# Performance work log

Measured on AMD Instinct MI355X. Metric: run time of the kernel, lower is better.

## Reference

```python
import jax, jax.numpy as jnp
import numpy as np

GR = 16

def _conv(x, w, b, pad):
    y = jax.lax.conv_general_dilated(x, w, (1, 1), [(pad, pad), (pad, pad)],
                                     dimension_numbers=('NCHW', 'OIHW', 'NCHW'))
    return y + b[None, :, None, None]

def _build_stencil(h, w):
    num = h * w
    a = np.zeros((num, 4, num), np.float32)
    i = np.arange(num)
    m0 = ((i + 1) % w != 0) & (i + 1 < num)
    a[i[m0], 0, i[m0]] = 1.0; a[i[m0], 0, i[m0] + 1] = -1.0
    m1 = i + w < num
    a[i[m1], 1, i[m1]] = 1.0; a[i[m1], 1, i[m1] + w] = -1.0
    m2 = ((i + 2) % w != 0) & (i + 2 < num)
    a[i[m2], 2, i[m2]] = 1.0; a[i[m2], 2, i[m2] + 2] = -1.0
    m3 = i + 2 * w < num
    a[i[m3], 3, i[m3]] = 1.0; a[i[m3], 3, i[m3] + 2 * w] = -1.0
    a[-1, 0, -1] = 1.0; a[-1, 1, -1] = 1.0; a[-1, 2, -1] = 1.0; a[-1, 3, -1] = 1.0
    return jnp.asarray(a)  # (num, 4, num)

def setup_inputs() -> dict:
    key = jax.random.key(0)
    ks = jax.random.split(key, 20)
    n, c, h, w = 4, 64, 24, 24
    s = 0.02
    inp = {
        'x': jax.random.normal(ks[0], (n, c, h, w), jnp.float32),
        'a': _build_stencil(h, w),
        'grad_w1': jax.random.normal(ks[1], (c, c, 3, 3)) * s,
        'grad_b1': jnp.zeros((c,)),
        'grad_w2': jax.random.normal(ks[2], (4 * GR, c, 3, 3)) * s,
        'grad_b2': jnp.zeros((4 * GR,)),
        'att_w1': jax.random.normal(ks[3], (c, c, 3, 3)) * s,
        'att_b1': jnp.zeros((c,)),
        'att_w2': jax.random.normal(ks[4], (4 * GR, c, 3, 3)) * s,
        'att_b2': jnp.zeros((4 * GR,)),
        'se_w1': jax.random.normal(ks[5], (c // 2, c, 1, 1)) * s,
        'se_b1': jnp.zeros((c // 2,)),
        'se_w2': jax.random.normal(ks[6], (GR, c // 2, 1, 1)) * s,
        'se_b2': jnp.zeros((GR,)),
        'gn_w': jnp.ones((GR,)),
        'gn_b': jnp.zeros((GR,)),
        'post_w': jax.random.normal(ks[7], (8 * GR, GR, 3, 3)) * s,
        'post_b': jnp.zeros((8 * GR,)),
    }
    return inp

def reference(x, a, grad_w1, grad_b1, grad_w2, grad_b2,
              att_w1, att_b1, att_w2, att_b2,
              se_w1, se_b1, se_w2, se_b2,
              gn_w, gn_b, post_w, post_b):
    n, c, h, w = x.shape
    num = h * w
    # attention branch: conv -> leaky_relu -> conv -> sigmoid
    att = jax.nn.sigmoid(_conv(jax.nn.leaky_relu(_conv(x, att_w1, att_b1, 1), 0.01), att_w2, att_b2, 1))
    # gradient branch: conv -> leaky_relu -> conv
    grad = _conv(jax.nn.leaky_relu(_conv(x, grad_w1, grad_b1, 1), 0.01), grad_w2, grad_b2, 1)
    # squeeze-excite: GAP -> 1x1 conv -> leaky -> 1x1 conv -> sigmoid
    pooled = x.mean(axis=(2, 3), keepdims=True)  # (n,c,1,1)
    se = jax.nn.sigmoid(_conv(jax.nn.leaky_relu(_conv(pooled, se_w1, se_b1, 0), 0.01), se_w2, se_b2, 0))
    # reshape per-pixel 4-tap weights: (n*GR, num, 4, 1)
    att_r = att.reshape(n * GR, 4, num, 1).transpose(0, 2, 1, 3)
    grad_r = grad.reshape(n * GR, 4, num, 1).transpose(0, 2, 1, 3)
    # densified weighted stencil operator
    A = a[None] * att_r                      # (b, num, 4, num)
    B = (grad_r * att_r)[..., 0]             # (b, num, 4)
    A = A.reshape(n * GR, num * 4, num)      # (b, 4num, num)
    B = B.reshape(n * GR, num * 4)           # (b, 4num)
    ATA = jnp.einsum('bkn,bkm->bnm', A, A)   # (b, num, num)
    ATB = jnp.einsum('bkn,bk->bn', A, B)[..., None]
    ATA = ATA + jnp.eye(num, dtype=x.dtype)[None] * 1e-12
    sol = jnp.linalg.solve(ATA, ATB)         # (b, num, 1)
    y = sol.reshape(n, GR, h, w)
    # GroupNorm(1, GR): normalize over all channels + spatial, eps=1e-5
    mu = y.mean(axis=(1, 2, 3), keepdims=True)
    var = y.var(axis=(1, 2, 3), keepdims=True)
    y = (y - mu) / jnp.sqrt(var + 1e-5)
    y = y * gn_w[None, :, None, None] + gn_b[None, :, None, None]
    y = se * y
    return _conv(y, post_w, post_b, 1)
```

## Files before the change

### kernel.cpp

```cpp
#include <hip/hip_runtime.h>
#include <math.h>

#define NUM 576
#define BSTR 50
#define CTH 512
#define CHOL_LDS_BYTES ((NUM * BSTR + CTH) * sizeof(float))

__device__ __forceinline__ float leakyf(float v) { return v > 0.f ? v : 0.01f * v; }
__device__ __forceinline__ float sigmoidf(float v) { return 1.f / (1.f + __expf(-v)); }
__device__ __forceinline__ float rdlane(float v, int l) {
  return __uint_as_float(__builtin_amdgcn_readlane(__float_as_uint(v), l));
}

__global__ __launch_bounds__(576) void conv1se_kernel(
    const float* __restrict__ x,
    const float* __restrict__ wa, const float* __restrict__ ba,
    const float* __restrict__ wg, const float* __restrict__ bg,
    const float* __restrict__ sw1, const float* __restrict__ sb1,
    const float* __restrict__ sw2, const float* __restrict__ sb2,
    float* __restrict__ outa, float* __restrict__ outg,
    float* __restrict__ sev, double* __restrict__ acc)
{
  __shared__ float sx[16 * 676];
  __shared__ float pooled[64];
  __shared__ float hid[32];
  const int co = blockIdx.x, n = blockIdx.y;
  const int tid = threadIdx.x;

  if (co == 64) {
    if (tid < 2) acc[n * 2 + tid] = 0.0;
    if (tid < 64) {
      const float4* xp4 = (const float4*)(x + (size_t)(n * 64 + tid) * 576);
      float s = 0.f;
      for (int p = 0; p < 144; ++p) {
        float4 v = xp4[p];
        s += v.x + v.y + v.z + v.w;
      }
      pooled[tid] = s * (1.f / 576.f);
    }
    __syncthreads();
    if (tid < 32) {
      float h = sb1[tid];
      for (int c = 0; c < 64; ++c) h += pooled[c] * sw1[tid * 64 + c];
      hid[tid] = leakyf(h);
    }
    __syncthreads();
    if (tid < 16) {
      float v = sb2[tid];
      for (int j = 0; j < 32; ++j) v += hid[j] * sw2[tid * 32 + j];
      sev[n * 16 + tid] = sigmoidf(v);
    }
    return;
  }

  const int py = tid / 24, px = tid - py * 24;
  const int hb0 = py * 26 + px;
  for (int i = tid; i < 16 * 676; i += 576) sx[i] = 0.f;
  float acc_a = ba[co];
  float acc_g = bg[co];
  for (int c0 = 0; c0 < 64; c0 += 16) {
    __syncthreads();
#pragma unroll
    for (int q = 0; q < 4; ++q) {
      const int p = tid + q * 576;
      const int k = p / 144;
      const int r = p - k * 144;
      const int pix = r * 4;
      const int ppy = pix / 24, ppx = pix - ppy * 24;
      const float4 v = *(const float4*)&x[(size_t)(n * 64 + c0) * 576 + p * 4];
      float* d = &sx[k * 676 + (ppy + 1) * 26 + ppx + 1];
      d[0] = v.x; d[1] = v.y; d[2] = v.z; d[3] = v.w;
    }
    __syncthreads();
#pragma unroll 4
    for (int k = 0; k < 16; ++k) {
      const float* wpa = wa + (co * 64 + c0 + k) * 9;
      const float* wpg = wg + (co * 64 + c0 + k) * 9;
      const float* sp = &sx[k * 676 + hb0];
#pragma unroll
      for (int dy = 0; dy < 3; ++dy)
#pragma unroll
        for (int dx = 0; dx < 3; ++dx) {
          const float v = sp[dy * 26 + dx];
          acc_a += v * wpa[dy * 3 + dx];
          acc_g += v * wpg[dy * 3 + dx];
        }
    }
  }
  const int o = (n * 64 + co) * 576 + tid;
  outa[o] = leakyf(acc_a);
  outg[o] = leakyf(acc_g);
}

__global__ __launch_bounds__(576) void conv2_kernel(
    const float* __restrict__ t1a, const float* __restrict__ t1g,
    const float* __restrict__ wa, const float* __restrict__ ba,
    const float* __restrict__ wg, const float* __restrict__ bg,
    float* __restrict__ att, float* __restrict__ grd)
{
  __shared__ float sx[16 * 676];
  const int co = blockIdx.x, n = blockIdx.y, br = blockIdx.z;
  const float* src = br ? t1g : t1a;
  const float* wp0 = br ? wg : wa;
  const float bias = br ? bg[co] : ba[co];
  float* dst = br ? grd : att;
  const int tid = threadIdx.x;
  const int py = tid / 24, px = tid - py * 24;
  const int hb0 = py * 26 + px;
  for (int i = tid; i < 16 * 676; i += 576) sx[i] = 0.f;
  float acc = bias;
  for (int c0 = 0; c0 < 64; c0 += 16) {
    __syncthreads();
#pragma unroll
    for (int q = 0; q < 4; ++q) {
      const int p = tid + q * 576;
      const int k = p / 144;
      const int r = p - k * 144;
      const int pix = r * 4;
      const int ppy = pix / 24, ppx = pix - ppy * 24;
      const float4 v = *(const float4*)&src[(size_t)(n * 64 + c0) * 576 + p * 4];
      float* d = &sx[k * 676 + (ppy + 1) * 26 + ppx + 1];
      d[0] = v.x; d[1] = v.y; d[2] = v.z; d[3] = v.w;
    }
    __syncthreads();
#pragma unroll 4
    for (int k = 0; k < 16; ++k) {
      const float* wp = wp0 + (co * 64 + c0 + k) * 9;
      const float* sp = &sx[k * 676 + hb0];
#pragma unroll
      for (int dy = 0; dy < 3; ++dy)
#pragma unroll
        for (int dx = 0; dx < 3; ++dx)
          acc += sp[dy * 26 + dx] * wp[dy * 3 + dx];
    }
  }
  if (br == 0) acc = sigmoidf(acc);
  dst[(n * 64 + co) * 576 + tid] = acc;
}

__device__ __forceinline__ void scale_panel_f(
    float* __restrict__ S, float* RHS_s, float* RD_s, float (*CP)[64],
    float* DUMW, int t, int j, int maxrow, int dumidx)
{
  const int row = j + t;
  const bool rok = row <= maxrow;
  float v[8];
#pragma unroll
  for (int c = 0; c < 8; ++c) {
    const bool okc = rok && (t >= c) && (t - c <= 48);
    const int addr = okc ? (row * BSTR + (t - c)) : dumidx;
    float vv = S[addr];
    v[c] = okc ? vv : 0.f;
  }
  float zb[8];
#pragma unroll
  for (int k = 0; k < 8; ++k) zb[k] = RHS_s[j + k];
  float z = RHS_s[rok ? row : j];
  z = rok ? z : 0.f;
  float rdv[8], y[8], lp[8][8];
#pragma unroll
  for (int k = 0; k < 8; ++k) {
    if (k == 0) rdv[0] = RD_s[j];
    else rdv[k] = rsqrtf(rdlane(v[k], k));
    v[k] *= rdv[k];
#pragma unroll
    for (int m = k + 1; m < 8; ++m) {
      lp[m][k] = rdlane(v[k], m);
      v[m] -= v[k] * lp[m][k];
    }
  }
  y[0] = zb[0] * rdv[0];
#pragma unroll
  for (int k = 1; k < 8; ++k) {
    float a = zb[k];
#pragma unroll
    for (int m = 0; m < 8; ++m)
      if (m < k) a -= lp[k][m] * y[m];
    y[k] = a * rdv[k];
  }
  float zn = z;
#pragma unroll
  for (int c = 0; c < 8; ++c) zn -= v[c] * y[c];
#pragma unroll
  for (int c = 0; c < 8; ++c) {
    const bool okc = rok && (t > c) && (t - c <= 48);
    float* bp = okc ? &S[row * BSTR + (t - c)] : &S[dumidx];
    *bp = v[c];
    CP[c][t] = okc ? v[c] : 0.f;
  }
  if (t < 8) {
    float yv = y[0], rv = rdv[0];
#pragma unroll
    for (int k = 1; k < 8; ++k) {
      yv = (t == k) ? y[k] : yv;
      rv = (t == k) ? rdv[k] : rv;
    }
    RHS_s[row] = yv;
    RD_s[row] = rv;
  } else {
    float* rp = rok ? &RHS_s[row] : &DUMW[t & 63];
    *rp = zn;
  }
}

__device__ __forceinline__ void scale_panel_b(
    float* __restrict__ S, float* RHS_s, float* RD_s, float (*CP)[64],
    float* DUMW, int t, int jf, int dumidx)
{
  const int rr = jf + t;
  const bool rok = rr <= 287;
  float v[8];
#pragma unroll
  for (int c = 0; c < 8; ++c) {
    const bool okc = rok && (t >= c) && (t - c <= 48);
    const int addr = okc ? ((575 - rr + (t - c)) * BSTR + (t - c)) : dumidx;
    float vv = S[addr];
    v[c] = okc ? vv : 0.f;
  }
  float zb[8];
#pragma unroll
  for (int k = 0; k < 8; ++k) zb[k] = RHS_s[575 - (jf + k)];
  float z = RHS_s[rok ? (575 - rr) : (575 - jf)];
  z = rok ? z : 0.f;
  float rdv[8], y[8], lp[8][8];
#pragma unroll
  for (int k = 0; k < 8; ++k) {
    if (k == 0) rdv[0] = RD_s[575 - jf];
    else rdv[k] = rsqrtf(rdlane(v[k], k));
    v[k] *= rdv[k];
#pragma unroll
    for (int m = k + 1; m < 8; ++m) {
      lp[m][k] = rdlane(v[k], m);
      v[m] -= v[k] * lp[m][k];
    }
  }
  y[0] = zb[0] * rdv[0];
#pragma unroll
  for (int k = 1; k < 8; ++k) {
    float a = zb[k];
#pragma unroll
    for (int m = 0; m < 8; ++m)
      if (m < k) a -= lp[k][m] * y[m];
    y[k] = a * rdv[k];
  }
  float zn = z;
#pragma unroll
  for (int c = 0; c < 8; ++c) zn -= v[c] * y[c];
#pragma unroll
  for (int c = 0; c < 8; ++c) {
    const bool okc = rok && (t > c) && (t - c <= 48);
    float* bp = okc ? &S[(575 - rr + (t - c)) * BSTR + (t - c)] : &S[dumidx];
    *bp = v[c];
    CP[c][t] = okc ? v[c] : 0.f;
  }
  if (t < 8) {
    float yv = y[0], rv = rdv[0];
#pragma unroll
    for (int k = 1; k < 8; ++k) {
      yv = (t == k) ? y[k] : yv;
      rv = (t == k) ? rdv[k] : rv;
    }
    RHS_s[575 - rr] = yv;
    RD_s[575 - rr] = rv;
  } else {
    float* rp = rok ? &RHS_s[575 - rr] : &DUMW[t & 63];
    *rp = zn;
  }
}

__global__ __launch_bounds__(CTH, 1) void chol_kernel(
    const float* __restrict__ att, const float* __restrict__ grd,
    float* __restrict__ sol, double* __restrict__ acc)
{
  extern __shared__ float S[];
  __shared__ float RHS_s[NUM];
  __shared__ float RD_s[NUM];
  __shared__ float XS_s[NUM];
  __shared__ __align__(16) float CPF[8][64];
  __shared__ __align__(16) float CPB[8][64];
  __shared__ float DUMW[64];
  __shared__ double RW[16];
  const int b = blockIdx.x, tid = threadIdx.x;
  const int n = b >> 4, g = b & 15;
  const float* ac = att + (size_t)(n * 64 + g * 4) * 576;
  const float* gc = grd + (size_t)(n * 64 + g * 4) * 576;
  const int dumidx = NUM * BSTR + tid;

  int r1A, r2A, r1B, r2B;
  const bool okA = tid < 300;
  const int btid = (tid >= 300) ? (tid - 300) : ((tid < 88) ? (tid + 212) : -1);
  const bool okB = btid >= 0;
  {
    int T = okA ? tid : 0;
    int U = (int)((sqrtf(8.f * (float)T + 1.f) - 1.f) * 0.5f);
    while (U * (U + 1) / 2 > T) --U;
    while ((U + 1) * (U + 2) / 2 <= T) ++U;
    int W = T - U * (U + 1) / 2;
    r1A = 8 + 2 * U; r2A = 8 + 2 * W;
    T = okB ? btid : 0;
    U = (int)((sqrtf(8.f * (float)T + 1.f) - 1.f) * 0.5f);
    while (U * (U + 1) / 2 > T) --U;
    while ((U + 1) * (U + 2) / 2 <= T) ++U;
    W = T - U * (U + 1) / 2;
    r1B = 8 + 2 * U; r2B = 8 + 2 * W;
  }

  for (int i = tid; i < NUM * BSTR; i += CTH) S[i] = 0.f;
  __syncthreads();

  for (int i = tid; i < NUM; i += CTH) {
    float diag = 1e-12f, rv = 0.f;
    float od1 = 0.f, od2 = 0.f, od24 = 0.f, od48 = 0.f;
    if (((i + 1) % 24 != 0) && (i + 1 < NUM)) {
      float a0 = ac[0 * 576 + i]; float s = a0 * a0;
      diag += s; rv += s * gc[0 * 576 + i];
    }
    if (i - 1 >= 0 && (i % 24 != 0)) {
      float a0 = ac[0 * 576 + (i - 1)]; float s = a0 * a0;
      diag += s; rv -= s * gc[0 * 576 + (i - 1)]; od1 = -s;
    }
    if (i + 24 < NUM) {
      float a1 = ac[1 * 576 + i]; float s = a1 * a1;
      diag += s; rv += s * gc[1 * 576 + i];
    }
    if (i - 24 >= 0) {
      float a1 = ac[1 * 576 + (i - 24)]; float s = a1 * a1;
      diag += s; rv -= s * gc[1 * 576 + (i - 24)]; od24 = -s;
    }
    if (((i + 2) % 24 != 0) && (i + 2 < NUM)) {
      float a2 = ac[2 * 576 + i]; float s = a2 * a2;
      diag += s; rv += s * gc[2 * 576 + i];
    }
    if (i - 2 >= 0 && (i % 24 != 0)) {
      float a2 = ac[2 * 576 + (i - 2)]; float s = a2 * a2;
      diag += s; rv -= s * gc[2 * 576 + (i - 2)]; od2 = -s;
    }
    if (i + 48 < NUM) {
      float a3 = ac[3 * 576 + i]; float s = a3 * a3;
      diag += s; rv += s * gc[3 * 576 + i];
    }
    if (i - 48 >= 0) {
      float a3 = ac[3 * 576 + (i - 48)]; float s = a3 * a3;
      diag += s; rv -= s * gc[3 * 576 + (i - 48)]; od48 = -s;
    }
    if (i == NUM - 1) {
#pragma unroll
      for (int t = 0; t < 4; ++t) {
        float a = ac[t * 576 + (NUM - 1)]; float s = a * a;
        diag += s; rv += s * gc[t * 576 + (NUM - 1)];
      }
    }
    S[i * BSTR + 0] = diag;
    S[i * BSTR + 1] = od1;
    S[i * BSTR + 2] = od2;
    S[i * BSTR + 24] = od24;
    S[i * BSTR + 48] = od48;
    RHS_s[i] = rv;
    if (i == 0) RD_s[0] = rsqrtf(diag);
    if (i == NUM - 1) RD_s[NUM - 1] = rsqrtf(diag);
  }

  for (int s = 0; s < 30; ++s) {
    const int j = 8 * s;
    __syncthreads();
    const int pF = j * BSTR + 51 * r1A - r2A;
    float* qF00 = okA ? &S[pF] : &S[dumidx];
    float* qF01 = okA ? &S[pF - 1] : &S[dumidx];
    float* qF10 = okA ? &S[pF + 51] : &S[dumidx];
    float* qF11 = okA ? &S[pF + 50] : &S[dumidx];
    const int pB = (575 - j - r2B) * BSTR + (r1B - r2B);
    float* qB00 = okB ? &S[pB] : &S[dumidx];
    float* qB01 = okB ? &S[pB - 51] : &S[dumidx];
    float* qB10 = okB ? &S[pB + 1] : &S[dumidx];
    float* qB11 = okB ? &S[pB - 50] : &S[dumidx];
    const float vF00 = *qF00, vF01 = *qF01, vF10 = *qF10, vF11 = *qF11;
    const float vB00 = *qB00, vB01 = *qB01, vB10 = *qB10, vB11 = *qB11;
    if (tid < 64)
      scale_panel_f(S, RHS_s, RD_s, CPF, DUMW, tid, j, 287, dumidx);
    else if (tid < 128)
      scale_panel_b(S, RHS_s, RD_s, CPB, DUMW, tid - 64, j, dumidx);
    __syncthreads();
    {
      float2 cr[8], cc[8];
#pragma unroll
      for (int c = 0; c < 8; ++c) {
        cr[c] = *(const float2*)&CPF[c][r1A];
        cc[c] = *(const float2*)&CPF[c][r2A];
      }
      float s00 = 0.f, s01 = 0.f, s10 = 0.f, s11 = 0.f;
#pragma unroll
      for (int c = 0; c < 8; ++c) {
        s00 += cr[c].x * cc[c].x; s01 += cr[c].x * cc[c].y;
        s10 += cr[c].y * cc[c].x; s11 += cr[c].y * cc[c].y;
      }
      const float t00 = vF00 - s00;
      *qF00 = t00; *qF01 = vF01 - s01;
      *qF10 = vF10 - s10; *qF11 = vF11 - s11;
      if (tid == 0) RD_s[j + 8] = rsqrtf(t00);
    }
    {
      float2 cr[8], cc[8];
#pragma unroll
      for (int c = 0; c < 8; ++c) {
        cr[c] = *(const float2*)&CPB[c][r1B];
        cc[c] = *(const float2*)&CPB[c][r2B];
      }
      float s00 = 0.f, s01 = 0.f, s10 = 0.f, s11 = 0.f;
#pragma unroll
      for (int c = 0; c < 8; ++c) {
        s00 += cr[c].x * cc[c].x; s01 += cr[c].x * cc[c].y;
        s10 += cr[c].y * cc[c].x; s11 += cr[c].y * cc[c].y;
      }
      const float t00 = vB00 - s00;
      *qB00 = t00; *qB01 = vB01 - s01;
      *qB10 = vB10 - s10; *qB11 = vB11 - s11;
      if (btid == 0 && j + 8 <= 239) RD_s[575 - (j + 8)] = rsqrtf(t00);
    }
  }

  for (int j = 240; j < 336; j += 8) {
    __syncthreads();
    const int R = 335 - j;
    const bool a0 = okA && (r1A <= R);
    const bool a1 = okA && (r1A + 1 <= R);
    const int pM = j * BSTR + 51 * r1A - r2A;
    float* qM00 = a0 ? &S[pM] : &S[dumidx];
    float* qM01 = a0 ? &S[pM - 1] : &S[dumidx];
    float* qM10 = a1 ? &S[pM + 51] : &S[dumidx];
    float* qM11 = a1 ? &S[pM + 50] : &S[dumidx];
    const float vM00 = *qM00, vM01 = *qM01, vM10 = *qM10, vM11 = *qM11;
    if (tid < 64)
      scale_panel_f(S, RHS_s, RD_s, CPF, DUMW, tid, j, 335, dumidx);
    __syncthreads();
    {
      float2 cr[8], cc[8];
#pragma unroll
      for (int c = 0; c < 8; ++c) {
        cr[c] = *(const float2*)&CPF[c][r1A];
        cc[c] = *(const float2*)&CPF[c][r2A];
      }
      float s00 = 0.f, s01 = 0.f, s10 = 0.f, s11 = 0.f;
#pragma unroll
      for (int c = 0; c < 8; ++c) {
        s00 += cr[c].x * cc[c].x; s01 += cr[c].x * cc[c].y;
        s10 += cr[c].y * cc[c].x; s11 += cr[c].y * cc[c].y;
      }
      const float t00 = vM00 - s00;
      *qM00 = t00; *qM01 = vM01 - s01;
      *qM10 = vM10 - s10; *qM11 = vM11 - s11;
      if (tid == 0 && a0) RD_s[j + 8] = rsqrtf(t00);
    }
  }
  __syncthreads();

  if (tid < 64) {
    const int t = tid;
    for (int i = 335; i >= 247; i -= 8) {
      asm volatile("s_waitcnt lgkmcnt(0)" ::: "memory");
      float zz[8], rr2[8];
#pragma unroll
      for (int k = 0; k < 8; ++k) { zz[k] = RHS_s[i - k]; rr2[k] = RD_s[i - k]; }
      float L[8][8];
#pragma unroll
      for (int a = 0; a < 8; ++a)
#pragma unroll
        for (int bb = 0; bb < 8; ++bb)
          if (bb > a) L[a][bb] = S[(i - a) * BSTR + (bb - a)];
      float x[8];
      x[0] = zz[0] * rr2[0];
#pragma unroll
      for (int k = 1; k < 8; ++k) {
        float a2 = zz[k];
#pragma unroll
        for (int m = 0; m < 8; ++m)
          if (m < k) a2 -= L[m][k] * x[m];
        x[k] = a2 * rr2[k];
      }
      const int rb = i - 8 - t;
      const bool bok = rb >= 0;
      float acc2 = 0.f;
#pragma unroll
      for (int k = 0; k < 8; ++k) {
        const int d = 8 + t - k;
        const bool ok = bok && (d <= 48);
        float Lv = S[ok ? ((i - k) * BSTR + d) : dumidx];
        Lv = ok ? Lv : 0.f;
        acc2 += Lv * x[k];
      }
      const float zbv = RHS_s[bok ? rb : 0];
      float* rp = bok ? &RHS_s[rb] : &DUMW[t];
      *rp = zbv - acc2;
      float xv = x[0];
#pragma unroll
      for (int k = 1; k < 8; ++k) xv = (t == k) ? x[k] : xv;
      if (t < 8) XS_s[i - t] = xv;
    }
  }
  __syncthreads();

  if (tid < 48) {
    const int jj = 336 + tid;
    float sacc = 0.f;
    for (int i = jj - 48; i <= 335; ++i)
      sacc += S[jj * BSTR + (jj - i)] * XS_s[i];
    RHS_s[jj] -= sacc;
  }
  __syncthreads();

  if (tid < 64) {
    const int t = tid;
    for (int i = 239; i >= 7; i -= 8) {
      asm volatile("s_waitcnt lgkmcnt(0)" ::: "memory");
      float zz[8], rr2[8];
#pragma unroll
      for (int k = 0; k < 8; ++k) { zz[k] = RHS_s[i - k]; rr2[k] = RD_s[i - k]; }
      float L[8][8];
#pragma unroll
      for (int a = 0; a < 8; ++a)
#pragma unroll
        for (int bb = 0; bb < 8; ++bb)
          if (bb > a) L[a][bb] = S[(i - a) * BSTR + (bb - a)];
      float x[8];
      x[0] = zz[0] * rr2[0];
#pragma unroll
      for (int k = 1; k < 8; ++k) {
        float a2 = zz[k];
#pragma unroll
        for (int m = 0; m < 8; ++m)
          if (m < k) a2 -= L[m][k] * x[m];
        x[k] = a2 * rr2[k];
      }
      const int rb = i - 8 - t;
      const bool bok = rb >= 0;
      float acc2 = 0.f;
#pragma unroll
      for (int k = 0; k < 8; ++k) {
        const int d = 8 + t - k;
        const bool ok = bok && (d <= 48);
        float Lv = S[ok ? ((i - k) * BSTR + d) : dumidx];
        Lv = ok ? Lv : 0.f;
        acc2 += Lv * x[k];
      }
      const float zbv = RHS_s[bok ? rb : 0];
      float* rp = bok ? &RHS_s[rb] : &DUMW[t];
      *rp = zbv - acc2;
      float xv = x[0];
#pragma unroll
      for (int k = 1; k < 8; ++k) xv = (t == k) ? x[k] : xv;
      if (t < 8) XS_s[i - t] = xv;
    }
  } else if (tid < 128) {
    const int t = tid - 64;
    for (int i = 239; i >= 7; i -= 8) {
      asm volatile("s_waitcnt lgkmcnt(0)" ::: "memory");
      float zz[8], rr2[8];
#pragma unroll
      for (int k = 0; k < 8; ++k) {
        zz[k] = RHS_s[575 - (i - k)];
        rr2[k] = RD_s[575 - (i - k)];
      }
      float L[8][8];
#pragma unroll
      for (int a = 0; a < 8; ++a)
#pragma unroll
        for (int bb = 0; bb < 8; ++bb)
          if (bb > a) L[a][bb] = S[(575 - (i - bb)) * BSTR + (bb - a)];
      float x[8];
      x[0] = zz[0] * rr2[0];
#pragma unroll
      for (int k = 1; k < 8; ++k) {
        float a2 = zz[k];
#pragma unroll
        for (int m = 0; m < 8; ++m)
          if (m < k) a2 -= L[m][k] * x[m];
        x[k] = a2 * rr2[k];
      }
      const int rb = i - 8 - t;
      const bool bok = rb >= 0;
      float acc2 = 0.f;
#pragma unroll
      for (int k = 0; k < 8; ++k) {
        const int d = 8 + t - k;
        const bool ok = bok && (d <= 48);
        float Lv = S[ok ? ((575 - rb) * BSTR + d) : dumidx];
        Lv = ok ? Lv : 0.f;
        acc2 += Lv * x[k];
      }
      const float zbv = RHS_s[bok ? (575 - rb) : 575];
      float* rp = bok ? &RHS_s[575 - rb] : &DUMW[t];
      *rp = zbv - acc2;
      float xv = x[0];
#pragma unroll
      for (int k = 1; k < 8; ++k) xv = (t == k) ? x[k] : xv;
      if (t < 8) XS_s[575 - (i - t)] = xv;
    }
  }
  __syncthreads();

  double ls = 0.0, ls2 = 0.0;
  for (int i = tid; i < NUM; i += CTH) {
    const float xv = XS_s[i];
    sol[(size_t)b * NUM + i] = xv;
    ls += (double)xv;
    ls2 += (double)xv * (double)xv;
  }
#pragma unroll
  for (int off = 32; off > 0; off >>= 1) {
    ls += __shfl_down(ls, off);
    ls2 += __shfl_down(ls2, off);
  }
  if ((tid & 63) == 0) {
    RW[(tid >> 6) * 2] = ls;
    RW[(tid >> 6) * 2 + 1] = ls2;
  }
  __syncthreads();
  if (tid == 0) {
    double s = 0.0, s2 = 0.0;
#pragma unroll
    for (int wv = 0; wv < 8; ++wv) { s += RW[wv * 2]; s2 += RW[wv * 2 + 1]; }
    atomicAdd(&acc[n * 2], s);
    atomicAdd(&acc[n * 2 + 1], s2);
  }
}

__global__ __launch_bounds__(576) void postgn_kernel(
    const float* __restrict__ sol, const double* __restrict__ acc,
    const float* __restrict__ sev,
    const float* __restrict__ gnw, const float* __restrict__ gnb,
    const float* __restrict__ w, const float* __restrict__ bias,
    float* __restrict__ out)
{
  __shared__ float sy[16 * 676];
  const int co = blockIdx.x, n = blockIdx.y, tid = threadIdx.x;
  const double mu_d = acc[n * 2] * (1.0 / 9216.0);
  const double var_d = acc[n * 2 + 1] * (1.0 / 9216.0) - mu_d * mu_d;
  const float rstd = (float)(1.0 / sqrt(var_d + 1e-5));
  const float muf = (float)mu_d;
  for (int i = tid; i < 16 * 676; i += 576) sy[i] = 0.f;
  __syncthreads();
#pragma unroll
  for (int q = 0; q < 4; ++q) {
    const int p = tid + q * 576;
    const int k = p / 144;
    const int r = p - k * 144;
    const int pix = r * 4;
    const int ppy = pix / 24, ppx = pix - ppy * 24;
    const float sv = sev[n * 16 + k];
    const float gw = gnw[k] * rstd;
    const float A = gw * sv;
    const float B = (gnb[k] - muf * gw) * sv;
    const float4 v = *(const float4*)&sol[(size_t)n * 9216 + p * 4];
    float* d = &sy[k * 676 + (ppy + 1) * 26 + ppx + 1];
    d[0] = v.x * A + B; d[1] = v.y * A + B;
    d[2] = v.z * A + B; d[3] = v.w * A + B;
  }
  __syncthreads();
  const int py = tid / 24, px = tid - py * 24;
  const int hb0 = py * 26 + px;
  float a = bias[co];
#pragma unroll 4
  for (int k = 0; k < 16; ++k) {
    const float* wp = w + (co * 16 + k) * 9;
    const float* sp = &sy[k * 676 + hb0];
#pragma unroll
    for (int dy = 0; dy < 3; ++dy)
#pragma unroll
      for (int dx = 0; dx < 3; ++dx)
        a += sp[dy * 26 + dx] * wp[dy * 3 + dx];
  }
  out[(size_t)(n * 128 + co) * 576 + tid] = a;
}

extern "C" void kernel_launch(void* const* d_in, const int* in_sizes, int n_in,
                              void* d_out, int out_size, void* d_ws, size_t ws_size,
                              hipStream_t stream) {
  const float* x       = (const float*)d_in[0];
  const float* grad_w1 = (const float*)d_in[2];
  const float* grad_b1 = (const float*)d_in[3];
  const float* grad_w2 = (const float*)d_in[4];
  const float* grad_b2 = (const float*)d_in[5];
  const float* att_w1  = (const float*)d_in[6];
  const float* att_b1  = (const float*)d_in[7];
  const float* att_w2  = (const float*)d_in[8];
  const float* att_b2  = (const float*)d_in[9];
  const float* se_w1   = (const float*)d_in[10];
  const float* se_b1   = (const float*)d_in[11];
  const float* se_w2   = (const float*)d_in[12];
  const float* se_b2   = (const float*)d_in[13];
  const float* gn_w    = (const float*)d_in[14];
  const float* gn_b    = (const float*)d_in[15];
  const float* post_w  = (const float*)d_in[16];
  const float* post_b  = (const float*)d_in[17];
  float* out = (float*)d_out;

  float* ws  = (float*)d_ws;
  float* t1a = ws;
  float* t1g = t1a + 147456;
  float* att = t1g + 147456;
  float* grd = att + 147456;
  float* sev = grd + 147456;
  float* sol = sev + 64;
  double* acc = (double*)(sol + 36864);

  (void)hipFuncSetAttribute((const void*)chol_kernel,
                            hipFuncAttributeMaxDynamicSharedMemorySize,
                            (int)CHOL_LDS_BYTES);

  conv1se_kernel<<<dim3(65, 4), 576, 0, stream>>>(
      x, att_w1, att_b1, grad_w1, grad_b1,
      se_w1, se_b1, se_w2, se_b2, t1a, t1g, sev, acc);
  conv2_kernel<<<dim3(64, 4, 2), 576, 0, stream>>>(t1a, t1g, att_w2, att_b2,
                                                   grad_w2, grad_b2, att, grd);
  chol_kernel<<<64, CTH, CHOL_LDS_BYTES, stream>>>(att, grd, sol, acc);
  postgn_kernel<<<dim3(128, 4), 576, 0, stream>>>(sol, acc, sev, gn_w, gn_b,
                                                  post_w, post_b, out);
}
```

Measured before the change: 170.6 us.

## Fuse all four stages into one cooperative persistent kernel with grid syncs

Replaces the four separate launches (conv1+SE, conv2, banded Cholesky solve, GroupNorm+post conv) with one cooperative kernel of 256 persistent blocks that loop over work units and use grid.sync between stages. The goal is to remove the launch overhead and inter-kernel gaps between the stages. In exchange, the conv stages now run with a fixed grid of 256 blocks at 576 threads and one block per CU because of launch bounds. Only 64 blocks do the solve while the others wait at the grid barrier, and grid-sync has its own cost.

Result: slower. 262.7 us (+54.0%).

```diff
diff --git a/kernel.cpp b/kernel.cpp
--- a/kernel.cpp
+++ b/kernel.cpp
@@ -1,141 +1,18 @@
 #include <hip/hip_runtime.h>
+#include <hip/hip_cooperative_groups.h>
 #include <math.h>
 
 #define NUM 576
 #define BSTR 50
-#define CTH 512
-#define CHOL_LDS_BYTES ((NUM * BSTR + CTH) * sizeof(float))
+#define NTH 576
+#define NBLK 256
+#define DYN_FLOATS (NUM * BSTR + NTH)
+#define DYN_BYTES (DYN_FLOATS * sizeof(float))
 
 __device__ __forceinline__ float leakyf(float v) { return v > 0.f ? v : 0.01f * v; }
 __device__ __forceinline__ float sigmoidf(float v) { return 1.f / (1.f + __expf(-v)); }
 __device__ __forceinline__ float rdlane(float v, int l) {
   return __uint_as_float(__builtin_amdgcn_readlane(__float_as_uint(v), l));
-}
-
-__global__ __launch_bounds__(576) void conv1se_kernel(
-    const float* __restrict__ x,
-    const float* __restrict__ wa, const float* __restrict__ ba,
-    const float* __restrict__ wg, const float* __restrict__ bg,
-    const float* __restrict__ sw1, const float* __restrict__ sb1,
-    const float* __restrict__ sw2, const float* __restrict__ sb2,
-    float* __restrict__ outa, float* __restrict__ outg,
-    float* __restrict__ sev, double* __restrict__ acc)
-{
-  __shared__ float sx[16 * 676];
-  __shared__ float pooled[64];
-  __shared__ float hid[32];
-  const int co = blockIdx.x, n = blockIdx.y;
-  const int tid = threadIdx.x;
-
-  if (co == 64) {
-    if (tid < 2) acc[n * 2 + tid] = 0.0;
-    if (tid < 64) {
-      const float4* xp4 = (const float4*)(x + (size_t)(n * 64 + tid) * 576);
-      float s = 0.f;
-      for (int p = 0; p < 144; ++p) {
-        float4 v = xp4[p];
-        s += v.x + v.y + v.z + v.w;
-      }
-      pooled[tid] = s * (1.f / 576.f);
-    }
-    __syncthreads();
-    if (tid < 32) {
-      float h = sb1[tid];
-      for (int c = 0; c < 64; ++c) h += pooled[c] * sw1[tid * 64 + c];
-      hid[tid] = leakyf(h);
-    }
-    __syncthreads();
-    if (tid < 16) {
-      float v = sb2[tid];
-      for (int j = 0; j < 32; ++j) v += hid[j] * sw2[tid * 32 + j];
-      sev[n * 16 + tid] = sigmoidf(v);
-    }
-    return;
-  }
-
-  const int py = tid / 24, px = tid - py * 24;
-  const int hb0 = py * 26 + px;
-  for (int i = tid; i < 16 * 676; i += 576) sx[i] = 0.f;
-  float acc_a = ba[co];
-  float acc_g = bg[co];
-  for (int c0 = 0; c0 < 64; c0 += 16) {
-    __syncthreads();
-#pragma unroll
-    for (int q = 0; q < 4; ++q) {
-      const int p = tid + q * 576;
-      const int k = p / 144;
-      const int r = p - k * 144;
-      const int pix = r * 4;
-      const int ppy = pix / 24, ppx = pix - ppy * 24;
-      const float4 v = *(const float4*)&x[(size_t)(n * 64 + c0) * 576 + p * 4];
-      float* d = &sx[k * 676 + (ppy + 1) * 26 + ppx + 1];
-      d[0] = v.x; d[1] = v.y; d[2] = v.z; d[3] = v.w;
-    }
-    __syncthreads();
-#pragma unroll 4
-    for (int k = 0; k < 16; ++k) {
-      const float* wpa = wa + (co * 64 + c0 + k) * 9;
-      const float* wpg = wg + (co * 64 + c0 + k) * 9;
-      const float* sp = &sx[k * 676 + hb0];
-#pragma unroll
-      for (int dy = 0; dy < 3; ++dy)
-#pragma unroll
-        for (int dx = 0; dx < 3; ++dx) {
-          const float v = sp[dy * 26 + dx];
-          acc_a += v * wpa[dy * 3 + dx];
-          acc_g += v * wpg[dy * 3 + dx];
-        }
-    }
-  }
-  const int o = (n * 64 + co) * 576 + tid;
-  outa[o] = leakyf(acc_a);
-  outg[o] = leakyf(acc_g);
-}
-
-__global__ __launch_bounds__(576) void conv2_kernel(
-    const float* __restrict__ t1a, const float* __restrict__ t1g,
-    const float* __restrict__ wa, const float* __restrict__ ba,
-    const float* __restrict__ wg, const float* __restrict__ bg,
-    float* __restrict__ att, float* __restrict__ grd)
-{
-  __shared__ float sx[16 * 676];
-  const int co = blockIdx.x, n = blockIdx.y, br = blockIdx.z;
-  const float* src = br ? t1g : t1a;
-  const float* wp0 = br ? wg : wa;
-  const float bias = br ? bg[co] : ba[co];
-  float* dst = br ? grd : att;
-  const int tid = threadIdx.x;
-  const int py = tid / 24, px = tid - py * 24;
-  const int hb0 = py * 26 + px;
-  for (int i = tid; i < 16 * 676; i += 576) sx[i] = 0.f;
-  float acc = bias;
-  for (int c0 = 0; c0 < 64; c0 += 16) {
-    __syncthreads();
-#pragma unroll
-    for (int q = 0; q < 4; ++q) {
-      const int p = tid + q * 576;
-      const int k = p / 144;
-      const int r = p - k * 144;
-      const int pix = r * 4;
-      const int ppy = pix / 24, ppx = pix - ppy * 24;
-      const float4 v = *(const float4*)&src[(size_t)(n * 64 + c0) * 576 + p * 4];
-      float* d = &sx[k * 676 + (ppy + 1) * 26 + ppx + 1];
-      d[0] = v.x; d[1] = v.y; d[2] = v.z; d[3] = v.w;
-    }
-    __syncthreads();
-#pragma unroll 4
-    for (int k = 0; k < 16; ++k) {
-      const float* wp = wp0 + (co * 64 + c0 + k) * 9;
-      const float* sp = &sx[k * 676 + hb0];
-#pragma unroll
-      for (int dy = 0; dy < 3; ++dy)
-#pragma unroll
-        for (int dx = 0; dx < 3; ++dx)
-          acc += sp[dy * 26 + dx] * wp[dy * 3 + dx];
-    }
-  }
-  if (br == 0) acc = sigmoidf(acc);
-  dst[(n * 64 + co) * 576 + tid] = acc;
 }
 
 __device__ __forceinline__ void scale_panel_f(
@@ -268,9 +145,20 @@
   }
 }
 
-__global__ __launch_bounds__(CTH, 1) void chol_kernel(
-    const float* __restrict__ att, const float* __restrict__ grd,
-    float* __restrict__ sol, double* __restrict__ acc)
+__global__ __launch_bounds__(NTH, 1) void fused_kernel(
+    const float* __restrict__ x,
+    const float* __restrict__ gw1, const float* __restrict__ gb1,
+    const float* __restrict__ gw2, const float* __restrict__ gb2,
+    const float* __restrict__ aw1, const float* __restrict__ ab1,
+    const float* __restrict__ aw2, const float* __restrict__ ab2,
+    const float* __restrict__ sw1, const float* __restrict__ sb1,
+    const float* __restrict__ sw2, const float* __restrict__ sb2,
+    const float* __restrict__ gnw, const float* __restrict__ gnb,
+    const float* __restrict__ pw, const float* __restrict__ pb,
+    float* __restrict__ t1a, float* __restrict__ t1g,
+    float* __restrict__ attb, float* __restrict__ grdb,
+    float* __restrict__ sev, float* __restrict__ sol,
+    double* __restrict__ acc, float* __restrict__ out)
 {
   extern __shared__ float S[];
   __shared__ float RHS_s[NUM];
@@ -279,396 +167,504 @@
   __shared__ __align__(16) float CPF[8][64];
   __shared__ __align__(16) float CPB[8][64];
   __shared__ float DUMW[64];
-  __shared__ double RW[16];
-  const int b = blockIdx.x, tid = threadIdx.x;
-  const int n = b >> 4, g = b & 15;
-  const float* ac = att + (size_t)(n * 64 + g * 4) * 576;
-  const float* gc = grd + (size_t)(n * 64 + g * 4) * 576;
-  const int dumidx = NUM * BSTR + tid;
-
-  int r1A, r2A, r1B, r2B;
-  const bool okA = tid < 300;
-  const int btid = (tid >= 300) ? (tid - 300) : ((tid < 88) ? (tid + 212) : -1);
-  const bool okB = btid >= 0;
-  {
-    int T = okA ? tid : 0;
-    int U = (int)((sqrtf(8.f * (float)T + 1.f) - 1.f) * 0.5f);
-    while (U * (U + 1) / 2 > T) --U;
-    while ((U + 1) * (U + 2) / 2 <= T) ++U;
-    int W = T - U * (U + 1) / 2;
-    r1A = 8 + 2 * U; r2A = 8 + 2 * W;
-    T = okB ? btid : 0;
-    U = (int)((sqrtf(8.f * (float)T + 1.f) - 1.f) * 0.5f);
-    while (U * (U + 1) / 2 > T) --U;
-    while ((U + 1) * (U + 2) / 2 <= T) ++U;
-    W = T - U * (U + 1) / 2;
-    r1B = 8 + 2 * U; r2B = 8 + 2 * W;
-  }
-
-  for (int i = tid; i < NUM * BSTR; i += CTH) S[i] = 0.f;
-  __syncthreads();
-
-  for (int i = tid; i < NUM; i += CTH) {
-    float diag = 1e-12f, rv = 0.f;
-    float od1 = 0.f, od2 = 0.f, od24 = 0.f, od48 = 0.f;
-    if (((i + 1) % 24 != 0) && (i + 1 < NUM)) {
-      float a0 = ac[0 * 576 + i]; float s = a0 * a0;
-      diag += s; rv += s * gc[0 * 576 + i];
-    }
-    if (i - 1 >= 0 && (i % 24 != 0)) {
-      float a0 = ac[0 * 576 + (i - 1)]; float s = a0 * a0;
-      diag += s; rv -= s * gc[0 * 576 + (i - 1)]; od1 = -s;
-    }
-    if (i + 24 < NUM) {
-      float a1 = ac[1 * 576 + i]; float s = a1 * a1;
-      diag += s; rv += s * gc[1 * 576 + i];
-    }
-    if (i - 24 >= 0) {
-      float a1 = ac[1 * 576 + (i - 24)]; float s = a1 * a1;
-      diag += s; rv -= s * gc[1 * 576 + (i - 24)]; od24 = -s;
-    }
-    if (((i + 2) % 24 != 0) && (i + 2 < NUM)) {
-      float a2 = ac[2 * 576 + i]; float s = a2 * a2;
-      diag += s; rv += s * gc[2 * 576 + i];
-    }
-    if (i - 2 >= 0 && (i % 24 != 0)) {
-      float a2 = ac[2 * 576 + (i - 2)]; float s = a2 * a2;
-      diag += s; rv -= s * gc[2 * 576 + (i - 2)]; od2 = -s;
-    }
-    if (i + 48 < NUM) {
-      float a3 = ac[3 * 576 + i]; float s = a3 * a3;
-      diag += s; rv += s * gc[3 * 576 + i];
-    }
-    if (i - 48 >= 0) {
-      float a3 = ac[3 * 576 + (i - 48)]; float s = a3 * a3;
-      diag += s; rv -= s * gc[3 * 576 + (i - 48)]; od48 = -s;
-    }
-    if (i == NUM - 1) {
-#pragma unroll
-      for (int t = 0; t < 4; ++t) {
-        float a = ac[t * 576 + (NUM - 1)]; float s = a * a;
-        diag += s; rv += s * gc[t * 576 + (NUM - 1)];
-      }
-    }
-    S[i * BSTR + 0] = diag;
-    S[i * BSTR + 1] = od1;
-    S[i * BSTR + 2] = od2;
-    S[i * BSTR + 24] = od24;
-    S[i * BSTR + 48] = od48;
-    RHS_s[i] = rv;
-    if (i == 0) RD_s[0] = rsqrtf(diag);
-    if (i == NUM - 1) RD_s[NUM - 1] = rsqrtf(diag);
-  }
-
-  for (int s = 0; s < 30; ++s) {
-    const int j = 8 * s;
-    __syncthreads();
-    const int pF = j * BSTR + 51 * r1A - r2A;
-    float* qF00 = okA ? &S[pF] : &S[dumidx];
-    float* qF01 = okA ? &S[pF - 1] : &S[dumidx];
-    float* qF10 = okA ? &S[pF + 51] : &S[dumidx];
-    float* qF11 = okA ? &S[pF + 50] : &S[dumidx];
-    const int pB = (575 - j - r2B) * BSTR + (r1B - r2B);
-    float* qB00 = okB ? &S[pB] : &S[dumidx];
-    float* qB01 = okB ? &S[pB - 51] : &S[dumidx];
-    float* qB10 = okB ? &S[pB + 1] : &S[dumidx];
-    float* qB11 = okB ? &S[pB - 50] : &S[dumidx];
-    const float vF00 = *qF00, vF01 = *qF01, vF10 = *qF10, vF11 = *qF11;
-    const float vB00 = *qB00, vB01 = *qB01, vB10 = *qB10, vB11 = *qB11;
-    if (tid < 64)
-      scale_panel_f(S, RHS_s, RD_s, CPF, DUMW, tid, j, 287, dumidx);
-    else if (tid < 128)
-      scale_panel_b(S, RHS_s, RD_s, CPB, DUMW, tid - 64, j, dumidx);
-    __syncthreads();
-    {
-      float2 cr[8], cc[8];
-#pragma unroll
-      for (int c = 0; c < 8; ++c) {
-        cr[c] = *(const float2*)&CPF[c][r1A];
-        cc[c] = *(const float2*)&CPF[c][r2A];
-      }
-      float s00 = 0.f, s01 = 0.f, s10 = 0.f, s11 = 0.f;
-#pragma unroll
-      for (int c = 0; c < 8; ++c) {
-        s00 += cr[c].x * cc[c].x; s01 += cr[c].x * cc[c].y;
-        s10 += cr[c].y * cc[c].x; s11 += cr[c].y * cc[c].y;
-      }
-      const float t00 = vF00 - s00;
-      *qF00 = t00; *qF01 = vF01 - s01;
-      *qF10 = vF10 - s10; *qF11 = vF11 - s11;
-      if (tid == 0) RD_s[j + 8] = rsqrtf(t00);
-    }
-    {
-      float2 cr[8], cc[8];
-#pragma unroll
-      for (int c = 0; c < 8; ++c) {
-        cr[c] = *(const float2*)&CPB[c][r1B];
-        cc[c] = *(const float2*)&CPB[c][r2B];
-      }
-      float s00 = 0.f, s01 = 0.f, s10 = 0.f, s11 = 0.f;
-#pragma unroll
-      for (int c = 0; c < 8; ++c) {
-        s00 += cr[c].x * cc[c].x; s01 += cr[c].x * cc[c].y;
-        s10 += cr[c].y * cc[c].x; s11 += cr[c].y * cc[c].y;
-      }
-      const float t00 = vB00 - s00;
-      *qB00 = t00; *qB01 = vB01 - s01;
-      *qB10 = vB10 - s10; *qB11 = vB11 - s11;
-      if (btid == 0 && j + 8 <= 239) RD_s[575 - (j + 8)] = rsqrtf(t00);
-    }
-  }
-
-  for (int j = 240; j < 336; j += 8) {
-    __syncthreads();
-    const int R = 335 - j;
-    const bool a0 = okA && (r1A <= R);
-    const bool a1 = okA && (r1A + 1 <= R);
-    const int pM = j * BSTR + 51 * r1A - r2A;
-    float* qM00 = a0 ? &S[pM] : &S[dumidx];
-    float* qM01 = a0 ? &S[pM - 1] : &S[dumidx];
-    float* qM10 = a1 ? &S[pM + 51] : &S[dumidx];
-    float* qM11 = a1 ? &S[pM + 50] : &S[dumidx];
-    const float vM00 = *qM00, vM01 = *qM01, vM10 = *qM10, vM11 = *qM11;
-    if (tid < 64)
-      scale_panel_f(S, RHS_s, RD_s, CPF, DUMW, tid, j, 335, dumidx);
-    __syncthreads();
-    {
-      float2 cr[8], cc[8];
-#pragma unroll
-      for (int c = 0; c < 8; ++c) {
-        cr[c] = *(const float2*)&CPF[c][r1A];
-        cc[c] = *(const float2*)&CPF[c][r2A];
-      }
-      float s00 = 0.f, s01 = 0.f, s10 = 0.f, s11 = 0.f;
-#pragma unroll
-      for (int c = 0; c < 8; ++c) {
-        s00 += cr[c].x * cc[c].x; s01 += cr[c].x * cc[c].y;
-        s10 += cr[c].y * cc[c].x; s11 += cr[c].y * cc[c].y;
-      }
-      const float t00 = vM00 - s00;
-      *qM00 = t00; *qM01 = vM01 - s01;
-      *qM10 = vM10 - s10; *qM11 = vM11 - s11;
-      if (tid == 0 && a0) RD_s[j + 8] = rsqrtf(t00);
-    }
-  }
-  __syncthreads();
-
-  if (tid < 64) {
-    const int t = tid;
-    for (int i = 335; i >= 247; i -= 8) {
-      asm volatile("s_waitcnt lgkmcnt(0)" ::: "memory");
-      float zz[8], rr2[8];
-#pragma unroll
-      for (int k = 0; k < 8; ++k) { zz[k] = RHS_s[i - k]; rr2[k] = RD_s[i - k]; }
-      float L[8][8];
-#pragma unroll
-      for (int a = 0; a < 8; ++a)
-#pragma unroll
-        for (int bb = 0; bb < 8; ++bb)
-          if (bb > a) L[a][bb] = S[(i - a) * BSTR + (bb - a)];
-      float x[8];
-      x[0] = zz[0] * rr2[0];
-#pragma unroll
-      for (int k = 1; k < 8; ++k) {
-        float a2 = zz[k];
-#pragma unroll
-        for (int m = 0; m < 8; ++m)
-          if (m < k) a2 -= L[m][k] * x[m];
-        x[k] = a2 * rr2[k];
-      }
-      const int rb = i - 8 - t;
-      const bool bok = rb >= 0;
-      float acc2 = 0.f;
-#pragma unroll
-      for (int k = 0; k < 8; ++k) {
-        const int d = 8 + t - k;
-        const bool ok = bok && (d <= 48);
-        float Lv = S[ok ? ((i - k) * BSTR + d) : dumidx];
-        Lv = ok ? Lv : 0.f;
-        acc2 += Lv * x[k];
-      }
-      const float zbv = RHS_s[bok ? rb : 0];
-      float* rp = bok ? &RHS_s[rb] : &DUMW[t];
-      *rp = zbv - acc2;
-      float xv = x[0];
-#pragma unroll
-      for (int k = 1; k < 8; ++k) xv = (t == k) ? x[k] : xv;
-      if (t < 8) XS_s[i - t] = xv;
-    }
-  }
-  __syncthreads();
-
-  if (tid < 48) {
-    const int jj = 336 + tid;
-    float sacc = 0.f;
-    for (int i = jj - 48; i <= 335; ++i)
-      sacc += S[jj * BSTR + (jj - i)] * XS_s[i];
-    RHS_s[jj] -= sacc;
-  }
-  __syncthreads();
-
-  if (tid < 64) {
-    const int t = tid;
-    for (int i = 239; i >= 7; i -= 8) {
-      asm volatile("s_waitcnt lgkmcnt(0)" ::: "memory");
-      float zz[8], rr2[8];
-#pragma unroll
-      for (int k = 0; k < 8; ++k) { zz[k] = RHS_s[i - k]; rr2[k] = RD_s[i - k]; }
-      float L[8][8];
-#pragma unroll
-      for (int a = 0; a < 8; ++a)
-#pragma unroll
-        for (int bb = 0; bb < 8; ++bb)
-          if (bb > a) L[a][bb] = S[(i - a) * BSTR + (bb - a)];
-      float x[8];
-      x[0] = zz[0] * rr2[0];
-#pragma unroll
-      for (int k = 1; k < 8; ++k) {
-        float a2 = zz[k];
-#pragma unroll
-        for (int m = 0; m < 8; ++m)
-          if (m < k) a2 -= L[m][k] * x[m];
-        x[k] = a2 * rr2[k];
-      }
-      const int rb = i - 8 - t;
-      const bool bok = rb >= 0;
-      float acc2 = 0.f;
-#pragma unroll
-      for (int k = 0; k < 8; ++k) {
-        const int d = 8 + t - k;
-        const bool ok = bok && (d <= 48);
-        float Lv = S[ok ? ((i - k) * BSTR + d) : dumidx];
-        Lv = ok ? Lv : 0.f;
-        acc2 += Lv * x[k];
-      }
-      const float zbv = RHS_s[bok ? rb : 0];
-      float* rp = bok ? &RHS_s[rb] : &DUMW[t];
-      *rp = zbv - acc2;
-      float xv = x[0];
-#pragma unroll
-      for (int k = 1; k < 8; ++k) xv = (t == k) ? x[k] : xv;
-      if (t < 8) XS_s[i - t] = xv;
-    }
-  } else if (tid < 128) {
-    const int t = tid - 64;
-    for (int i = 239; i >= 7; i -= 8) {
-      asm volatile("s_waitcnt lgkmcnt(0)" ::: "memory");
-      float zz[8], rr2[8];
-#pragma unroll
-      for (int k = 0; k < 8; ++k) {
-        zz[k] = RHS_s[575 - (i - k)];
-        rr2[k] = RD_s[575 - (i - k)];
-      }
-      float L[8][8];
-#pragma unroll
-      for (int a = 0; a < 8; ++a)
-#pragma unroll
-        for (int bb = 0; bb < 8; ++bb)
-          if (bb > a) L[a][bb] = S[(575 - (i - bb)) * BSTR + (bb - a)];
-      float x[8];
-      x[0] = zz[0] * rr2[0];
-#pragma unroll
-      for (int k = 1; k < 8; ++k) {
-        float a2 = zz[k];
-#pragma unroll
-        for (int m = 0; m < 8; ++m)
-          if (m < k) a2 -= L[m][k] * x[m];
-        x[k] = a2 * rr2[k];
-      }
-      const int rb = i - 8 - t;
-      const bool bok = rb >= 0;
-      float acc2 = 0.f;
-#pragma unroll
-      for (int k = 0; k < 8; ++k) {
-        const int d = 8 + t - k;
-        const bool ok = bok && (d <= 48);
-        float Lv = S[ok ? ((575 - rb) * BSTR + d) : dumidx];
-        Lv = ok ? Lv : 0.f;
-        acc2 += Lv * x[k];
-      }
-      const float zbv = RHS_s[bok ? (575 - rb) : 575];
-      float* rp = bok ? &RHS_s[575 - rb] : &DUMW[t];
-      *rp = zbv - acc2;
-      float xv = x[0];
-#pragma unroll
-      for (int k = 1; k < 8; ++k) xv = (t == k) ? x[k] : xv;
-      if (t < 8) XS_s[575 - (i - t)] = xv;
-    }
-  }
-  __syncthreads();
-
-  double ls = 0.0, ls2 = 0.0;
-  for (int i = tid; i < NUM; i += CTH) {
-    const float xv = XS_s[i];
-    sol[(size_t)b * NUM + i] = xv;
-    ls += (double)xv;
-    ls2 += (double)xv * (double)xv;
-  }
-#pragma unroll
-  for (int off = 32; off > 0; off >>= 1) {
-    ls += __shfl_down(ls, off);
-    ls2 += __shfl_down(ls2, off);
-  }
-  if ((tid & 63) == 0) {
-    RW[(tid >> 6) * 2] = ls;
-    RW[(tid >> 6) * 2 + 1] = ls2;
-  }
-  __syncthreads();
-  if (tid == 0) {
-    double s = 0.0, s2 = 0.0;
-#pragma unroll
-    for (int wv = 0; wv < 8; ++wv) { s += RW[wv * 2]; s2 += RW[wv * 2 + 1]; }
-    atomicAdd(&acc[n * 2], s);
-    atomicAdd(&acc[n * 2 + 1], s2);
-  }
-}
-
-__global__ __launch_bounds__(576) void postgn_kernel(
-    const float* __restrict__ sol, const double* __restrict__ acc,
-    const float* __restrict__ sev,
-    const float* __restrict__ gnw, const float* __restrict__ gnb,
-    const float* __restrict__ w, const float* __restrict__ bias,
-    float* __restrict__ out)
-{
-  __shared__ float sy[16 * 676];
-  const int co = blockIdx.x, n = blockIdx.y, tid = threadIdx.x;
-  const double mu_d = acc[n * 2] * (1.0 / 9216.0);
-  const double var_d = acc[n * 2 + 1] * (1.0 / 9216.0) - mu_d * mu_d;
-  const float rstd = (float)(1.0 / sqrt(var_d + 1e-5));
-  const float muf = (float)mu_d;
-  for (int i = tid; i < 16 * 676; i += 576) sy[i] = 0.f;
-  __syncthreads();
-#pragma unroll
-  for (int q = 0; q < 4; ++q) {
-    const int p = tid + q * 576;
-    const int k = p / 144;
-    const int r = p - k * 144;
-    const int pix = r * 4;
-    const int ppy = pix / 24, ppx = pix - ppy * 24;
-    const float sv = sev[n * 16 + k];
-    const float gw = gnw[k] * rstd;
-    const float A = gw * sv;
-    const float B = (gnb[k] - muf * gw) * sv;
-    const float4 v = *(const float4*)&sol[(size_t)n * 9216 + p * 4];
-    float* d = &sy[k * 676 + (ppy + 1) * 26 + ppx + 1];
-    d[0] = v.x * A + B; d[1] = v.y * A + B;
-    d[2] = v.z * A + B; d[3] = v.w * A + B;
-  }
-  __syncthreads();
+  __shared__ double RW[18];
+  __shared__ float pooled[64];
+  __shared__ float hid[32];
+  cooperative_groups::grid_group grid = cooperative_groups::this_grid();
+  const int bid = blockIdx.x, tid = threadIdx.x;
   const int py = tid / 24, px = tid - py * 24;
   const int hb0 = py * 26 + px;
-  float a = bias[co];
+
+  for (int u = bid; u < 260; u += NBLK) {
+    const int n = u / 65, co = u % 65;
+    __syncthreads();
+    if (co == 64) {
+      if (tid < 2) acc[n * 2 + tid] = 0.0;
+      if (tid < 64) {
+        const float4* xp4 = (const float4*)(x + (size_t)(n * 64 + tid) * 576);
+        float s = 0.f;
+        for (int p = 0; p < 144; ++p) {
+          float4 v = xp4[p];
+          s += v.x + v.y + v.z + v.w;
+        }
+        pooled[tid] = s * (1.f / 576.f);
+      }
+      __syncthreads();
+      if (tid < 32) {
+        float h = sb1[tid];
+        for (int c = 0; c < 64; ++c) h += pooled[c] * sw1[tid * 64 + c];
+        hid[tid] = leakyf(h);
+      }
+      __syncthreads();
+      if (tid < 16) {
+        float v = sb2[tid];
+        for (int jj = 0; jj < 32; ++jj) v += hid[jj] * sw2[tid * 32 + jj];
+        sev[n * 16 + tid] = sigmoidf(v);
+      }
+    } else {
+      for (int i = tid; i < 16 * 676; i += NTH) S[i] = 0.f;
+      float acc_a = ab1[co];
+      float acc_g = gb1[co];
+      for (int c0 = 0; c0 < 64; c0 += 16) {
+        __syncthreads();
+#pragma unroll
+        for (int q = 0; q < 4; ++q) {
+          const int p = tid + q * 576;
+          const int k = p / 144;
+          const int r = p - k * 144;
+          const int pix = r * 4;
+          const int ppy = pix / 24, ppx = pix - ppy * 24;
+          const float4 v = *(const float4*)&x[(size_t)(n * 64 + c0) * 576 + p * 4];
+          float* d = &S[k * 676 + (ppy + 1) * 26 + ppx + 1];
+          d[0] = v.x; d[1] = v.y; d[2] = v.z; d[3] = v.w;
+        }
+        __syncthreads();
 #pragma unroll 4
-  for (int k = 0; k < 16; ++k) {
-    const float* wp = w + (co * 16 + k) * 9;
-    const float* sp = &sy[k * 676 + hb0];
-#pragma unroll
-    for (int dy = 0; dy < 3; ++dy)
-#pragma unroll
-      for (int dx = 0; dx < 3; ++dx)
-        a += sp[dy * 26 + dx] * wp[dy * 3 + dx];
-  }
-  out[(size_t)(n * 128 + co) * 576 + tid] = a;
+        for (int k = 0; k < 16; ++k) {
+          const float* wpa = aw1 + (co * 64 + c0 + k) * 9;
+          const float* wpg = gw1 + (co * 64 + c0 + k) * 9;
+          const float* sp = &S[k * 676 + hb0];
+#pragma unroll
+          for (int dy = 0; dy < 3; ++dy)
+#pragma unroll
+            for (int dx = 0; dx < 3; ++dx) {
+              const float v = sp[dy * 26 + dx];
+              acc_a += v * wpa[dy * 3 + dx];
+              acc_g += v * wpg[dy * 3 + dx];
+            }
+        }
+      }
+      const int o = (n * 64 + co) * 576 + tid;
+      t1a[o] = leakyf(acc_a);
+      t1g[o] = leakyf(acc_g);
+    }
+  }
+  grid.sync();
+
+  for (int u = bid; u < 512; u += NBLK) {
+    const int co = u & 63, n = (u >> 6) & 3, br = u >> 8;
+    __syncthreads();
+    const float* src = br ? t1g : t1a;
+    const float* wp0 = br ? gw2 : aw2;
+    const float bias = br ? gb2[co] : ab2[co];
+    float* dst = br ? grdb : attb;
+    for (int i = tid; i < 16 * 676; i += NTH) S[i] = 0.f;
+    float a = bias;
+    for (int c0 = 0; c0 < 64; c0 += 16) {
+      __syncthreads();
+#pragma unroll
+      for (int q = 0; q < 4; ++q) {
+        const int p = tid + q * 576;
+        const int k = p / 144;
+        const int r = p - k * 144;
+        const int pix = r * 4;
+        const int ppy = pix / 24, ppx = pix - ppy * 24;
+        const float4 v = *(const float4*)&src[(size_t)(n * 64 + c0) * 576 + p * 4];
+        float* d = &S[k * 676 + (ppy + 1) * 26 + ppx + 1];
+        d[0] = v.x; d[1] = v.y; d[2] = v.z; d[3] = v.w;
+      }
+      __syncthreads();
+#pragma unroll 4
+      for (int k = 0; k < 16; ++k) {
+        const float* wp = wp0 + (co * 64 + c0 + k) * 9;
+        const float* sp = &S[k * 676 + hb0];
+#pragma unroll
+        for (int dy = 0; dy < 3; ++dy)
+#pragma unroll
+          for (int dx = 0; dx < 3; ++dx)
+            a += sp[dy * 26 + dx] * wp[dy * 3 + dx];
+      }
+    }
+    if (br == 0) a = sigmoidf(a);
+    dst[(n * 64 + co) * 576 + tid] = a;
+  }
+  grid.sync();
+
+  if (bid < 64) {
+    const int b = bid;
+    const int n = b >> 4, g = b & 15;
+    const float* ac = attb + (size_t)(n * 64 + g * 4) * 576;
+    const float* gc = grdb + (size_t)(n * 64 + g * 4) * 576;
+    const int dumidx = NUM * BSTR + tid;
+
+    int r1A, r2A, r1B, r2B;
+    const bool okA = tid < 300;
+    const int btid = (tid >= 300) ? (tid - 300) : ((tid < 24) ? (tid + 276) : -1);
+    const bool okB = btid >= 0;
+    {
+      int T = okA ? tid : 0;
+      int U = (int)((sqrtf(8.f * (float)T + 1.f) - 1.f) * 0.5f);
+      while (U * (U + 1) / 2 > T) --U;
+      while ((U + 1) * (U + 2) / 2 <= T) ++U;
+      int W = T - U * (U + 1) / 2;
+      r1A = 8 + 2 * U; r2A = 8 + 2 * W;
+      T = okB ? btid : 0;
+      U = (int)((sqrtf(8.f * (float)T + 1.f) - 1.f) * 0.5f);
+      while (U * (U + 1) / 2 > T) --U;
+      while ((U + 1) * (U + 2) / 2 <= T) ++U;
+      W = T - U * (U + 1) / 2;
+      r1B = 8 + 2 * U; r2B = 8 + 2 * W;
+    }
+
+    __syncthreads();
+    for (int i = tid; i < NUM * BSTR; i += NTH) S[i] = 0.f;
+    __syncthreads();
+
+    for (int i = tid; i < NUM; i += NTH) {
+      float diag = 1e-12f, rv = 0.f;
+      float od1 = 0.f, od2 = 0.f, od24 = 0.f, od48 = 0.f;
+      if (((i + 1) % 24 != 0) && (i + 1 < NUM)) {
+        float a0 = ac[0 * 576 + i]; float s = a0 * a0;
+        diag += s; rv += s * gc[0 * 576 + i];
+      }
+      if (i - 1 >= 0 && (i % 24 != 0)) {
+        float a0 = ac[0 * 576 + (i - 1)]; float s = a0 * a0;
+        diag += s; rv -= s * gc[0 * 576 + (i - 1)]; od1 = -s;
+      }
+      if (i + 24 < NUM) {
+        float a1 = ac[1 * 576 + i]; float s = a1 * a1;
+        diag += s; rv += s * gc[1 * 576 + i];
+      }
+      if (i - 24 >= 0) {
+        float a1 = ac[1 * 576 + (i - 24)]; float s = a1 * a1;
+        diag += s; rv -= s * gc[1 * 576 + (i - 24)]; od24 = -s;
+      }
+      if (((i + 2) % 24 != 0) && (i + 2 < NUM)) {
+        float a2 = ac[2 * 576 + i]; float s = a2 * a2;
+        diag += s; rv += s * gc[2 * 576 + i];
+      }
+      if (i - 2 >= 0 && (i % 24 != 0)) {
+        float a2 = ac[2 * 576 + (i - 2)]; float s = a2 * a2;
+        diag += s; rv -= s * gc[2 * 576 + (i - 2)]; od2 = -s;
+      }
+      if (i + 48 < NUM) {
+        float a3 = ac[3 * 576 + i]; float s = a3 * a3;
+        diag += s; rv += s * gc[3 * 576 + i];
+      }
+      if (i - 48 >= 0) {
+        float a3 = ac[3 * 576 + (i - 48)]; float s = a3 * a3;
+        diag += s; rv -= s * gc[3 * 576 + (i - 48)]; od48 = -s;
+      }
+      if (i == NUM - 1) {
+#pragma unroll
+        for (int t = 0; t < 4; ++t) {
+          float a = ac[t * 576 + (NUM - 1)]; float s = a * a;
+          diag += s; rv += s * gc[t * 576 + (NUM - 1)];
+        }
+      }
+      S[i * BSTR + 0] = diag;
+      S[i * BSTR + 1] = od1;
+      S[i * BSTR + 2] = od2;
+      S[i * BSTR + 24] = od24;
+      S[i * BSTR + 48] = od48;
+      RHS_s[i] = rv;
+      if (i == 0) RD_s[0] = rsqrtf(diag);
+      if (i == NUM - 1) RD_s[NUM - 1] = rsqrtf(diag);
+    }
+
+    for (int s = 0; s < 30; ++s) {
+      const int j = 8 * s;
+      __syncthreads();
+      const int pF = j * BSTR + 51 * r1A - r2A;
+      float* qF00 = okA ? &S[pF] : &S[dumidx];
+      float* qF01 = okA ? &S[pF - 1] : &S[dumidx];
+      float* qF10 = okA ? &S[pF + 51] : &S[dumidx];
+      float* qF11 = okA ? &S[pF + 50] : &S[dumidx];
+      const int pB = (575 - j - r2B) * BSTR + (r1B - r2B);
+      float* qB00 = okB ? &S[pB] : &S[dumidx];
+      float* qB01 = okB ? &S[pB - 51] : &S[dumidx];
+      float* qB10 = okB ? &S[pB + 1] : &S[dumidx];
+      float* qB11 = okB ? &S[pB - 50] : &S[dumidx];
+      const float vF00 = *qF00, vF01 = *qF01, vF10 = *qF10, vF11 = *qF11;
+      const float vB00 = *qB00, vB01 = *qB01, vB10 = *qB10, vB11 = *qB11;
+      if (tid < 64)
+        scale_panel_f(S, RHS_s, RD_s, CPF, DUMW, tid, j, 287, dumidx);
+      else if (tid < 128)
+        scale_panel_b(S, RHS_s, RD_s, CPB, DUMW, tid - 64, j, dumidx);
+      __syncthreads();
+      {
+        float2 cr[8], cc[8];
+#pragma unroll
+        for (int c = 0; c < 8; ++c) {
+          cr[c] = *(const float2*)&CPF[c][r1A];
+          cc[c] = *(const float2*)&CPF[c][r2A];
+        }
+        float s00 = 0.f, s01 = 0.f, s10 = 0.f, s11 = 0.f;
+#pragma unroll
+        for (int c = 0; c < 8; ++c) {
+          s00 += cr[c].x * cc[c].x; s01 += cr[c].x * cc[c].y;
+          s10 += cr[c].y * cc[c].x; s11 += cr[c].y * cc[c].y;
+        }
+        const float t00 = vF00 - s00;
+        *qF00 = t00; *qF01 = vF01 - s01;
+        *qF10 = vF10 - s10; *qF11 = vF11 - s11;
+        if (tid == 0) RD_s[j + 8] = rsqrtf(t00);
+      }
+      {
+        float2 cr[8], cc[8];
+#pragma unroll
+        for (int c = 0; c < 8; ++c) {
+          cr[c] = *(const float2*)&CPB[c][r1B];
+          cc[c] = *(const float2*)&CPB[c][r2B];
+        }
+        float s00 = 0.f, s01 = 0.f, s10 = 0.f, s11 = 0.f;
+#pragma unroll
+        for (int c = 0; c < 8; ++c) {
+          s00 += cr[c].x * cc[c].x; s01 += cr[c].x * cc[c].y;
+          s10 += cr[c].y * cc[c].x; s11 += cr[c].y * cc[c].y;
+        }
+        const float t00 = vB00 - s00;
+        *qB00 = t00; *qB01 = vB01 - s01;
+        *qB10 = vB10 - s10; *qB11 = vB11 - s11;
+        if (btid == 0 && j + 8 <= 239) RD_s[575 - (j + 8)] = rsqrtf(t00);
+      }
+    }
+
+    for (int j = 240; j < 336; j += 8) {
+      __syncthreads();
+      const int R = 335 - j;
+      const bool a0 = okA && (r1A <= R);
+      const bool a1 = okA && (r1A + 1 <= R);
+      const int pM = j * BSTR + 51 * r1A - r2A;
+      float* qM00 = a0 ? &S[pM] : &S[dumidx];
+      float* qM01 = a0 ? &S[pM - 1] : &S[dumidx];
+      float* qM10 = a1 ? &S[pM + 51] : &S[dumidx];
+      float* qM11 = a1 ? &S[pM + 50] : &S[dumidx];
+      const float vM00 = *qM00, vM01 = *qM01, vM10 = *qM10, vM11 = *qM11;
+      if (tid < 64)
+        scale_panel_f(S, RHS_s, RD_s, CPF, DUMW, tid, j, 335, dumidx);
+      __syncthreads();
+      {
+        float2 cr[8], cc[8];
+#pragma unroll
+        for (int c = 0; c < 8; ++c) {
+          cr[c] = *(const float2*)&CPF[c][r1A];
+          cc[c] = *(const float2*)&CPF[c][r2A];
+        }
+        float s00 = 0.f, s01 = 0.f, s10 = 0.f, s11 = 0.f;
+#pragma unroll
+        for (int c = 0; c < 8; ++c) {
+          s00 += cr[c].x * cc[c].x; s01 += cr[c].x * cc[c].y;
+          s10 += cr[c].y * cc[c].x; s11 += cr[c].y * cc[c].y;
+        }
+        const float t00 = vM00 - s00;
+        *qM00 = t00; *qM01 = vM01 - s01;
+        *qM10 = vM10 - s10; *qM11 = vM11 - s11;
+        if (tid == 0 && a0) RD_s[j + 8] = rsqrtf(t00);
+      }
+    }
+    __syncthreads();
+
+    if (tid < 64) {
+      const int t = tid;
+      for (int i = 335; i >= 247; i -= 8) {
+        asm volatile("s_waitcnt lgkmcnt(0)" ::: "memory");
+        float zz[8], rr2[8];
+#pragma unroll
+        for (int k = 0; k < 8; ++k) { zz[k] = RHS_s[i - k]; rr2[k] = RD_s[i - k]; }
+        float L[8][8];
+#pragma unroll
+        for (int a = 0; a < 8; ++a)
+#pragma unroll
+          for (int bb = 0; bb < 8; ++bb)
+            if (bb > a) L[a][bb] = S[(i - a) * BSTR + (bb - a)];
+        float xx[8];
+        xx[0] = zz[0] * rr2[0];
+#pragma unroll
+        for (int k = 1; k < 8; ++k) {
+          float a2 = zz[k];
+#pragma unroll
+          for (int m = 0; m < 8; ++m)
+            if (m < k) a2 -= L[m][k] * xx[m];
+          xx[k] = a2 * rr2[k];
+        }
+        const int rb = i - 8 - t;
+        const bool bok = rb >= 0;
+        float acc2 = 0.f;
+#pragma unroll
+        for (int k = 0; k < 8; ++k) {
+          const int d = 8 + t - k;
+          const bool ok = bok && (d <= 48);
+          float Lv = S[ok ? ((i - k) * BSTR + d) : dumidx];
+          Lv = ok ? Lv : 0.f;
+          acc2 += Lv * xx[k];
+        }
+        const float zbv = RHS_s[bok ? rb : 0];
+        float* rp = bok ? &RHS_s[rb] : &DUMW[t];
+        *rp = zbv - acc2;
+        float xv = xx[0];
+#pragma unroll
+        for (int k = 1; k < 8; ++k) xv = (t == k) ? xx[k] : xv;
+        if (t < 8) XS_s[i - t] = xv;
+      }
+    }
+    __syncthreads();
+
+    if (tid < 48) {
+      const int jj = 336 + tid;
+      float sacc = 0.f;
+      for (int i = jj - 48; i <= 335; ++i)
+        sacc += S[jj * BSTR + (jj - i)] * XS_s[i];
+      RHS_s[jj] -= sacc;
+    }
+    __syncthreads();
+
+    if (tid < 64) {
+      const int t = tid;
+      for (int i = 239; i >= 7; i -= 8) {
+        asm volatile("s_waitcnt lgkmcnt(0)" ::: "memory");
+        float zz[8], rr2[8];
+#pragma unroll
+        for (int k = 0; k < 8; ++k) { zz[k] = RHS_s[i - k]; rr2[k] = RD_s[i - k]; }
+        float L[8][8];
+#pragma unroll
+        for (int a = 0; a < 8; ++a)
+#pragma unroll
+          for (int bb = 0; bb < 8; ++bb)
+            if (bb > a) L[a][bb] = S[(i - a) * BSTR + (bb - a)];
+        float xx[8];
+        xx[0] = zz[0] * rr2[0];
+#pragma unroll
+        for (int k = 1; k < 8; ++k) {
+          float a2 = zz[k];
+#pragma unroll
+          for (int m = 0; m < 8; ++m)
+            if (m < k) a2 -= L[m][k] * xx[m];
+          xx[k] = a2 * rr2[k];
+        }
+        const int rb = i - 8 - t;
+        const bool bok = rb >= 0;
+        float acc2 = 0.f;
+#pragma unroll
+        for (int k = 0; k < 8; ++k) {
+          const int d = 8 + t - k;
+          const bool ok = bok && (d <= 48);
+          float Lv = S[ok ? ((i - k) * BSTR + d) : dumidx];
+          Lv = ok ? Lv : 0.f;
+          acc2 += Lv * xx[k];
+        }
+        const float zbv = RHS_s[bok ? rb : 0];
+        float* rp = bok ? &RHS_s[rb] : &DUMW[t];
+        *rp = zbv - acc2;
+        float xv = xx[0];
+#pragma unroll
+        for (int k = 1; k < 8; ++k) xv = (t == k) ? xx[k] : xv;
+        if (t < 8) XS_s[i - t] = xv;
+      }
+    } else if (tid < 128) {
+      const int t = tid - 64;
+      for (int i = 239; i >= 7; i -= 8) {
+        asm volatile("s_waitcnt lgkmcnt(0)" ::: "memory");
+        float zz[8], rr2[8];
+#pragma unroll
+        for (int k = 0; k < 8; ++k) {
+          zz[k] = RHS_s[575 - (i - k)];
+          rr2[k] = RD_s[575 - (i - k)];
+        }
+        float L[8][8];
+#pragma unroll
+        for (int a = 0; a < 8; ++a)
+#pragma unroll
+          for (int bb = 0; bb < 8; ++bb)
+            if (bb > a) L[a][bb] = S[(575 - (i - bb)) * BSTR + (bb - a)];
+        float xx[8];
+        xx[0] = zz[0] * rr2[0];
+#pragma unroll
+        for (int k = 1; k < 8; ++k) {
+          float a2 = zz[k];
+#pragma unroll
+          for (int m = 0; m < 8; ++m)
+            if (m < k) a2 -= L[m][k] * xx[m];
+          xx[k] = a2 * rr2[k];
+        }
+        const int rb = i - 8 - t;
+        const bool bok = rb >= 0;
+        float acc2 = 0.f;
+#pragma unroll
+        for (int k = 0; k < 8; ++k) {
+          const int d = 8 + t - k;
+          const bool ok = bok && (d <= 48);
+          float Lv = S[ok ? ((575 - rb) * BSTR + d) : dumidx];
+          Lv = ok ? Lv : 0.f;
+          acc2 += Lv * xx[k];
+        }
+        const float zbv = RHS_s[bok ? (575 - rb) : 575];
+        float* rp = bok ? &RHS_s[575 - rb] : &DUMW[t];
+        *rp = zbv - acc2;
+        float xv = xx[0];
+#pragma unroll
+        for (int k = 1; k < 8; ++k) xv = (t == k) ? xx[k] : xv;
+        if (t < 8) XS_s[575 - (i - t)] = xv;
+      }
+    }
+    __syncthreads();
+
+    double ls = 0.0, ls2 = 0.0;
+    for (int i = tid; i < NUM; i += NTH) {
+      const float xv = XS_s[i];
+      sol[(size_t)b * NUM + i] = xv;
+      ls += (double)xv;
+      ls2 += (double)xv * (double)xv;
+    }
+#pragma unroll
+    for (int off = 32; off > 0; off >>= 1) {
+      ls += __shfl_down(ls, off);
+      ls2 += __shfl_down(ls2, off);
+    }
+    if ((tid & 63) == 0) {
+      RW[(tid >> 6) * 2] = ls;
+      RW[(tid >> 6) * 2 + 1] = ls2;
+    }
+    __syncthreads();
+    if (tid == 0) {
+      double s = 0.0, s2 = 0.0;
+#pragma unroll
+      for (int wv = 0; wv < 9; ++wv) { s += RW[wv * 2]; s2 += RW[wv * 2 + 1]; }
+      atomicAdd(&acc[n * 2], s);
+      atomicAdd(&acc[n * 2 + 1], s2);
+    }
+  }
+  grid.sync();
+
+  for (int u = bid; u < 512; u += NBLK) {
+    const int co = u & 127, n = u >> 7;
+    __syncthreads();
+    const double mu_d = acc[n * 2] * (1.0 / 9216.0);
+    const double var_d = acc[n * 2 + 1] * (1.0 / 9216.0) - mu_d * mu_d;
+    const float rstd = (float)(1.0 / sqrt(var_d + 1e-5));
+    const float muf = (float)mu_d;
+    for (int i = tid; i < 16 * 676; i += NTH) S[i] = 0.f;
+    __syncthreads();
+#pragma unroll
+    for (int q = 0; q < 4; ++q) {
+      const int p = tid + q * 576;
+      const int k = p / 144;
+      const int r = p - k * 144;
+      const int pix = r * 4;
+      const int ppy = pix / 24, ppx = pix - ppy * 24;
+      const float sv = sev[n * 16 + k];
+      const float gwv = gnw[k] * rstd;
+      const float A = gwv * sv;
+      const float B = (gnb[k] - muf * gwv) * sv;
+      const float4 v = *(const float4*)&sol[(size_t)n * 9216 + p * 4];
+      float* d = &S[k * 676 + (ppy + 1) * 26 + ppx + 1];
+      d[0] = v.x * A + B; d[1] = v.y * A + B;
+      d[2] = v.z * A + B; d[3] = v.w * A + B;
+    }
+    __syncthreads();
+    float a = pb[co];
+#pragma unroll 4
+    for (int k = 0; k < 16; ++k) {
+      const float* wp = pw + (co * 16 + k) * 9;
+      const float* sp = &S[k * 676 + hb0];
+#pragma unroll
+      for (int dy = 0; dy < 3; ++dy)
+#pragma unroll
+        for (int dx = 0; dx < 3; ++dx)
+          a += sp[dy * 26 + dx] * wp[dy * 3 + dx];
+    }
+    out[(size_t)(n * 128 + co) * 576 + tid] = a;
+  }
 }
 
 extern "C" void kernel_launch(void* const* d_in, const int* in_sizes, int n_in,
@@ -702,16 +698,19 @@
   float* sol = sev + 64;
   double* acc = (double*)(sol + 36864);
 
-  (void)hipFuncSetAttribute((const void*)chol_kernel,
+  (void)hipFuncSetAttribute((const void*)fused_kernel,
                             hipFuncAttributeMaxDynamicSharedMemorySize,
-                            (int)CHOL_LDS_BYTES);
-
-  conv1se_kernel<<<dim3(65, 4), 576, 0, stream>>>(
-      x, att_w1, att_b1, grad_w1, grad_b1,
-      se_w1, se_b1, se_w2, se_b2, t1a, t1g, sev, acc);
-  conv2_kernel<<<dim3(64, 4, 2), 576, 0, stream>>>(t1a, t1g, att_w2, att_b2,
-                                                   grad_w2, grad_b2, att, grd);
-  chol_kernel<<<64, CTH, CHOL_LDS_BYTES, stream>>>(att, grd, sol, acc);
-  postgn_kernel<<<dim3(128, 4), 576, 0, stream>>>(sol, acc, sev, gn_w, gn_b,
-                                                  post_w, post_b, out);
+                            (int)DYN_BYTES);
+
+  void* args[] = {
+      (void*)&x,
+      (void*)&grad_w1, (void*)&grad_b1, (void*)&grad_w2, (void*)&grad_b2,
+      (void*)&att_w1,  (void*)&att_b1,  (void*)&att_w2,  (void*)&att_b2,
+      (void*)&se_w1,   (void*)&se_b1,   (void*)&se_w2,   (void*)&se_b2,
+      (void*)&gn_w,    (void*)&gn_b,    (void*)&post_w,  (void*)&post_b,
+      (void*)&t1a, (void*)&t1g, (void*)&att, (void*)&grd,
+      (void*)&sev, (void*)&sol, (void*)&acc, (void*)&out};
+  (void)hipLaunchCooperativeKernel((const void*)fused_kernel, dim3(NBLK),
+                                   dim3(NTH), args, (unsigned)DYN_BYTES,
+                                   stream);
 }
```
